# Performance work log

Hardware: AMD Instinct MI355X
Metric: run time of the kernel (lower is better)

Reference implementation:

```python
import jax, jax.numpy as jnp
import numpy as np

HEAD_COUNT = 16
HEAD_DIM = 128  # embed_count // head_count = 2048 // 16


def setup_inputs() -> dict:
    key = jax.random.key(0)
    k0, k1, k2, k3, k4 = jax.random.split(key, 5)
    B, C, S = 4, 2048, 1024
    keys = jax.random.normal(k0, (B, C, 1, S), dtype=jnp.float32)
    values = jax.random.normal(k1, (B, C, 1, S), dtype=jnp.float32)
    queries = jax.random.normal(k2, (B, C, 1, S), dtype=jnp.float32)
    attention_mask = jax.random.randint(k3, (B, S), 0, 2).astype(bool)
    # guarantee at least one valid key per batch row so softmax is finite
    attention_mask = attention_mask.at[:, 0].set(True)
    w_out = jax.random.normal(k4, (C, C), dtype=jnp.float32) * 0.02
    return {"keys": keys, "values": values, "queries": queries,
            "attention_mask": attention_mask, "w_out": w_out}


def reference(keys, values, queries, attention_mask, w_out):
    B, C, _, S = keys.shape
    h, d = HEAD_COUNT, HEAD_DIM
    # keys: [B,C,1,S] -> transpose(1,3) -> [B,S,1,C] -> [B,S,h,d]
    k = jnp.transpose(keys[:, :, 0, :], (0, 2, 1)).reshape(B, S, h, d)      # bkhd
    # values/queries: [B,C,1,S] -> [B,h,d,S] -> transpose(1,2) -> [B,d,h,S]
    v = jnp.transpose(values[:, :, 0, :].reshape(B, h, d, S), (0, 2, 1, 3))  # bdhk
    q = jnp.transpose(queries[:, :, 0, :].reshape(B, h, d, S), (0, 2, 1, 3)) # bdhq
    # additive mask bias: 0 where attended, -inf where masked; broadcast over h,q
    bias = jnp.where(attention_mask, 0.0, -jnp.inf).astype(keys.dtype)       # [B,K]
    scale = 1.0 / np.sqrt(d).astype(np.float32)
    w = jnp.einsum('bdhq,bkhd->bkhq', q * scale, k)                          # [B,K,h,Q]
    w = w + bias[:, :, None, None]
    w = jax.nn.softmax(w, axis=1)  # softmax over keys (dim 1)
    hid = jnp.einsum('bkhq,bdhk->bdhq', w, v)                                # [B,d,h,Q]
    hid = jnp.transpose(hid, (0, 2, 1, 3)).reshape(B, C, S)                  # [B,C,Q]
    out = jnp.einsum('oc,bcq->boq', w_out, hid)                              # 1x1 conv out_proj
    return out.reshape(B, C, 1, S)
```

## Files before the change

### kernel.cpp

```cpp
#include <hip/hip_runtime.h>

#define Bq 4
#define Cc 2048
#define Ss 1024
#define Hh 16
#define Dd 128

#define QSCALE 0.127517429f

typedef __bf16 bf16x8 __attribute__((ext_vector_type(8)));
typedef float  f32x4  __attribute__((ext_vector_type(4)));

__device__ __forceinline__ ushort f2bf(float f) {
    uint u = __float_as_uint(f);
    u += 0x7FFFu + ((u >> 16) & 1u);
    return (ushort)(u >> 16);
}
__device__ __forceinline__ uint pack2bf(float a, float b) {
    return (uint)f2bf(a) | ((uint)f2bf(b) << 16);
}
__device__ __forceinline__ void gld16(const void* g, void* l) {
    __builtin_amdgcn_global_load_lds(
        (const __attribute__((address_space(1))) unsigned int*)g,
        (__attribute__((address_space(3))) unsigned int*)l, 16, 0, 0);
}

__global__ __launch_bounds__(256) void prep_all(const float* __restrict__ w,
                                                const float* __restrict__ v,
                                                const float* __restrict__ keys,
                                                ushort* __restrict__ wb,
                                                ushort* __restrict__ vb,
                                                ushort* __restrict__ Kt) {
    __shared__ __align__(16) float T[128][65];
    const int t = threadIdx.x;
    const int blk = blockIdx.x;

    if (blk < 2048) {
        const size_t e = ((size_t)blk * 256 + t) * 8;
        const int row = (int)(e >> 11), col = (int)(e & 2047);
        const int colS = (col & ~63) | ((col & 63) ^ ((row & 7) << 3));
        float4 v0 = *(const float4*)&w[e];
        float4 v1 = *(const float4*)&w[e + 4];
        uint4 o;
        o.x = pack2bf(v0.x, v0.y); o.y = pack2bf(v0.z, v0.w);
        o.z = pack2bf(v1.x, v1.y); o.w = pack2bf(v1.z, v1.w);
        *(uint4*)&wb[(size_t)row * 2048 + colS] = o;
    } else if (blk < 6144) {
        const int tid = (blk - 2048) * 256 + t;
        const int row = tid >> 7;
        const int cp = tid & 127;
        const int blk64 = (cp >> 3) * 64;
        const int j0 = cp & 7;
        const int b5 = j0 >> 2, h = j0 & 3;
        const float* src = v + (size_t)row * 1024 + blk64 + 32 * b5 + 4 * h;
        float4 A = *(const float4*)src;
        float4 B = *(const float4*)(src + 16);
        uint4 o;
        o.x = pack2bf(A.x, A.y); o.y = pack2bf(A.z, A.w);
        o.z = pack2bf(B.x, B.y); o.w = pack2bf(B.z, B.w);
        *(uint4*)&vb[(size_t)row * 1024 + blk64 + ((j0 * 8) ^ ((row & 7) << 3))] = o;
    } else {
        const int b2 = blk - 6144;
        const int s0 = (b2 & 15) * 64;
        const int bh = b2 >> 4;
        const float* src = keys + (size_t)bh * 128 * 1024;
#pragma unroll
        for (int p = 0; p < 8; ++p) {
            const int d = p * 16 + (t >> 4);
            float4 v4 = *(const float4*)&src[(size_t)d * 1024 + s0 + (t & 15) * 4];
            T[d][(t & 15) * 4 + 0] = v4.x;
            T[d][(t & 15) * 4 + 1] = v4.y;
            T[d][(t & 15) * 4 + 2] = v4.z;
            T[d][(t & 15) * 4 + 3] = v4.w;
        }
        __syncthreads();
#pragma unroll
        for (int p = 0; p < 4; ++p) {
            const int k = p * 16 + (t >> 4);
            const int x = t & 15;
            uint4 o;
            o.x = pack2bf(T[x * 8 + 0][k], T[x * 8 + 1][k]);
            o.y = pack2bf(T[x * 8 + 2][k], T[x * 8 + 3][k]);
            o.z = pack2bf(T[x * 8 + 4][k], T[x * 8 + 5][k]);
            o.w = pack2bf(T[x * 8 + 6][k], T[x * 8 + 7][k]);
            const size_t rowbyte = ((size_t)bh * 1024 + s0 + k) * 256;
            const int boff = (x * 16) ^ ((k & 7) << 4);
            *(uint4*)((char*)Kt + rowbyte + boff) = o;
        }
    }
}

__global__ __launch_bounds__(512, 2) void attn7(const float* __restrict__ queries,
                                                const ushort* __restrict__ Kt,
                                                const ushort* __restrict__ Vbf,
                                                const unsigned* __restrict__ mask,
                                                ushort* __restrict__ hidT) {
    __shared__ __align__(16) char SMEM[102416];
    float* biasS = (float*)(SMEM + 98304);
    int* flg = (int*)(SMEM + 102400);

    const int t = threadIdx.x, l = t & 63, w = t >> 6;
    const int kk = l & 15, g = l >> 4;

    const int bid = blockIdx.x;
    const int vid = (bid & 7) * 32 + (bid >> 3);
    const int bh = vid >> 2, qt = vid & 3;
    const int b = bh >> 4, hh = bh & 15;
    const int q0 = qt * 256;
    const size_t bhbase = (size_t)bh * 1024;

    if (t == 0) { flg[0] = 0; flg[1] = 0; }
    __syncthreads();
    {
        int a = 0, c = 0;
        for (int i = t; i < 1024; i += 512) {
            unsigned vv = mask[i];
            if (vv != 0u && vv != 1u) a = 1;
            if (vv != 0u && vv != 0x3F800000u) c = 1;
        }
        if (a) atomicOr(&flg[0], 1);
        if (c) atomicOr(&flg[1], 1);
        __syncthreads();
        const int mode = flg[0] ? (flg[1] ? 1 : 2) : 0;
        const int* mi = (const int*)mask;
        const unsigned char* mb = (const unsigned char*)mask;
        const float* mf = (const float*)mask;
        for (int i = t; i < 1024; i += 512) {
            bool on;
            if (mode == 0)      on = (mi[b * 1024 + i] != 0);
            else if (mode == 1) on = (mb[b * 1024 + i] != 0);
            else                on = (mf[b * 1024 + i] != 0.0f);
            biasS[i] = on ? 0.0f : -1e30f;
        }
    }

    const float* Qb = queries + ((size_t)(b * Cc + hh * Dd)) * Ss;
    bf16x8 qf[2][4];
#pragma unroll
    for (int qs = 0; qs < 2; ++qs)
#pragma unroll
        for (int dc = 0; dc < 4; ++dc) {
            const int q = q0 + w * 32 + qs * 16 + kk;
            float v0 = Qb[(size_t)(dc * 32 + g * 8 + 0) * Ss + q];
            float v1 = Qb[(size_t)(dc * 32 + g * 8 + 1) * Ss + q];
            float v2 = Qb[(size_t)(dc * 32 + g * 8 + 2) * Ss + q];
            float v3 = Qb[(size_t)(dc * 32 + g * 8 + 3) * Ss + q];
            float v4 = Qb[(size_t)(dc * 32 + g * 8 + 4) * Ss + q];
            float v5 = Qb[(size_t)(dc * 32 + g * 8 + 5) * Ss + q];
            float v6 = Qb[(size_t)(dc * 32 + g * 8 + 6) * Ss + q];
            float v7 = Qb[(size_t)(dc * 32 + g * 8 + 7) * Ss + q];
            uint4 u;
            u.x = pack2bf(v0 * QSCALE, v1 * QSCALE);
            u.y = pack2bf(v2 * QSCALE, v3 * QSCALE);
            u.z = pack2bf(v4 * QSCALE, v5 * QSCALE);
            u.w = pack2bf(v6 * QSCALE, v7 * QSCALE);
            qf[qs][dc] = *(bf16x8*)&u;
        }

    float lrun[2] = {0.0f, 0.0f};
    f32x4 hacc[2][8];
#pragma unroll
    for (int qs = 0; qs < 2; ++qs)
#pragma unroll
        for (int i = 0; i < 8; ++i) hacc[qs][i] = (f32x4){0.f, 0.f, 0.f, 0.f};

#define ATTN_STAGE(bufi, cki)                                                   \
    {                                                                           \
        const int k0n = (cki) * 64;                                             \
        ushort* Kd = (ushort*)SMEM + (bufi) * 8192;                             \
        ushort* Vd = (ushort*)(SMEM + 49152) + (bufi) * 8192;                   \
        _Pragma("unroll")                                                       \
        for (int ii = 0; ii < 4; ++ii) {                                        \
            const int inst = ii * 8 + w;                                        \
            if (inst < 16) {                                                    \
                gld16(Kt + (bhbase + k0n + inst * 4 + (l >> 4)) * 128 +         \
                          (l & 15) * 8,                                         \
                      Kd + inst * 512);                                         \
            } else {                                                            \
                const int i2 = inst - 16;                                       \
                gld16(Vbf + ((size_t)bh * 128 + i2 * 8 + (l >> 3)) * 1024 +     \
                          k0n + (l & 7) * 8,                                    \
                      Vd + i2 * 512);                                           \
            }                                                                   \
        }                                                                       \
    }

#define ATTN_COMPUTE(bi, ck)                                                     \
    {                                                                            \
        const int k0 = (ck) * 64;                                                \
        const ushort* KTb = (const ushort*)SMEM + (bi) * 8192;                   \
        const ushort* Vsb = (const ushort*)(SMEM + 49152) + (bi) * 8192;         \
        f32x4 sc[2][4];                                                          \
        __builtin_amdgcn_s_setprio(1);                                           \
        _Pragma("unroll")                                                        \
        for (int ns = 0; ns < 4; ++ns) {                                         \
            const f32x4 ci = *(const f32x4*)&biasS[k0 + ns * 16 + g * 4];        \
            bf16x8 kf[4];                                                        \
            const ushort* kr = KTb + (ns * 16 + kk) * 128;                       \
            _Pragma("unroll")                                                    \
            for (int dc = 0; dc < 4; ++dc)                                       \
                kf[dc] = *(const bf16x8*)(kr +                                   \
                             ((dc * 32 + g * 8) ^ ((kk & 7) << 3)));             \
            _Pragma("unroll")                                                    \
            for (int qs = 0; qs < 2; ++qs) {                                     \
                f32x4 a = ci;                                                    \
                _Pragma("unroll")                                                \
                for (int dc = 0; dc < 4; ++dc)                                   \
                    a = __builtin_amdgcn_mfma_f32_16x16x32_bf16(                 \
                        kf[dc], qf[qs][dc], a, 0, 0, 0);                         \
                sc[qs][ns] = a;                                                  \
            }                                                                    \
        }                                                                        \
        __builtin_amdgcn_s_setprio(0);                                           \
        bf16x8 pb[2][2];                                                         \
        _Pragma("unroll")                                                        \
        for (int qs = 0; qs < 2; ++qs) {                                         \
            float pv[4][4];                                                      \
            float s = 0.0f;                                                      \
            _Pragma("unroll")                                                    \
            for (int ns = 0; ns < 4; ++ns) {                                     \
                _Pragma("unroll")                                                \
                for (int r = 0; r < 4; ++r) {                                    \
                    float p = exp2f(sc[qs][ns][r]);                              \
                    pv[ns][r] = p;                                               \
                    s += p;                                                      \
                }                                                                \
            }                                                                    \
            lrun[qs] += s;                                                       \
            _Pragma("unroll")                                                    \
            for (int kh = 0; kh < 2; ++kh) {                                     \
                bf16x8 vpk;                                                      \
                _Pragma("unroll")                                                \
                for (int j = 0; j < 8; ++j)                                      \
                    vpk[j] = (__bf16)pv[2 * kh + (j >> 2)][j & 3];               \
                pb[qs][kh] = vpk;                                                \
            }                                                                    \
        }                                                                        \
        __builtin_amdgcn_s_setprio(1);                                           \
        _Pragma("unroll")                                                        \
        for (int kh = 0; kh < 2; ++kh) {                                         \
            _Pragma("unroll")                                                    \
            for (int ds = 0; ds < 8; ++ds) {                                     \
                bf16x8 vf = *(const bf16x8*)(Vsb + (ds * 16 + kk) * 64 +         \
                                 ((kh * 32 + g * 8) ^ ((kk & 7) << 3)));         \
                hacc[0][ds] = __builtin_amdgcn_mfma_f32_16x16x32_bf16(           \
                    vf, pb[0][kh], hacc[0][ds], 0, 0, 0);                        \
                hacc[1][ds] = __builtin_amdgcn_mfma_f32_16x16x32_bf16(           \
                    vf, pb[1][kh], hacc[1][ds], 0, 0, 0);                        \
            }                                                                    \
        }                                                                        \
        __builtin_amdgcn_s_setprio(0);                                           \
    }

    ATTN_STAGE(0, 0);
    ATTN_STAGE(1, 1);
    asm volatile("s_waitcnt vmcnt(4)" ::: "memory");
    __builtin_amdgcn_s_barrier();

    int cb = 0, sb = 2;
    for (int ck = 0; ck < 14; ++ck) {
        ATTN_STAGE(sb, ck + 2);
        ATTN_COMPUTE(cb, ck);
        asm volatile("s_waitcnt vmcnt(4)" ::: "memory");
        __builtin_amdgcn_s_barrier();
        cb = (cb == 2) ? 0 : cb + 1;
        sb = (sb == 2) ? 0 : sb + 1;
    }
    ATTN_COMPUTE(cb, 14);
    asm volatile("s_waitcnt vmcnt(0)" ::: "memory");
    __builtin_amdgcn_s_barrier();
    cb = (cb == 2) ? 0 : cb + 1;
    ATTN_COMPUTE(cb, 15);
#undef ATTN_STAGE
#undef ATTN_COMPUTE

    float linv[2];
#pragma unroll
    for (int qs = 0; qs < 2; ++qs) {
        float s = lrun[qs];
        s += __shfl_xor(s, 16);
        s += __shfl_xor(s, 32);
        linv[qs] = 1.0f / s;
    }

    __syncthreads();
    {
        ushort* hs = (ushort*)SMEM;
#pragma unroll
        for (int qs = 0; qs < 2; ++qs) {
            const int row = w * 32 + qs * 16 + kk;
#pragma unroll
            for (int ds = 0; ds < 8; ++ds) {
                uint2 pk;
                pk.x = pack2bf(hacc[qs][ds][0] * linv[qs], hacc[qs][ds][1] * linv[qs]);
                pk.y = pack2bf(hacc[qs][ds][2] * linv[qs], hacc[qs][ds][3] * linv[qs]);
                const int off = row * 256 + ((ds * 32 + g * 8) ^ ((row & 7) << 4));
                *(uint2*)((char*)hs + off) = pk;
            }
        }
    }
    __syncthreads();

    const char* hsb = (const char*)SMEM;
#pragma unroll
    for (int it = 0; it < 8; ++it) {
        const int idx = it * 512 + t;
        const int q = idx >> 4, x = idx & 15;
        uint4 vv = *(const uint4*)(hsb + q * 256 + x * 16);
        *(uint4*)((char*)hidT + ((size_t)(b * Ss + q0 + q)) * 4096 + hh * 256 + x * 16) = vv;
    }
}

__global__ __launch_bounds__(512, 2) void proj5(const ushort* __restrict__ Wbf,
                                                const ushort* __restrict__ hidT,
                                                float* __restrict__ out) {
    __shared__ __align__(16) char SMEM[147456];
    const int t = threadIdx.x, l = t & 63, w = t >> 6;
    const int kk = l & 15, g = l >> 4;
    const int wr = w >> 2, wc = w & 3;

    const int bid = blockIdx.x;
    const int vid = (bid & 7) * 32 + (bid >> 3);
    const int o0 = (vid & 15) * 128;
    const int n0 = (vid >> 4) * 256;

    f32x4 acc[4][4];
#pragma unroll
    for (int i = 0; i < 4; ++i)
#pragma unroll
        for (int j = 0; j < 4; ++j) acc[i][j] = (f32x4){0.f, 0.f, 0.f, 0.f};

    const int swz = (kk & 7) << 3;

#define P5_STAGE_A(st, ks)                                                      \
    {                                                                           \
        ushort* Ad = (ushort*)SMEM + (st) * 8192;                               \
        _Pragma("unroll")                                                       \
        for (int ii = 0; ii < 2; ++ii) {                                        \
            const int idx = ii * 512 + t;                                       \
            gld16(Wbf + (size_t)(o0 + (idx >> 3)) * 2048 + (ks) * 64 +          \
                      (idx & 7) * 8,                                            \
                  Ad + idx * 8);                                                \
        }                                                                       \
    }
#define P5_STAGE_B(st, ks, p)                                                   \
    {                                                                           \
        ushort* Bd = (ushort*)(SMEM + 49152) + (st) * 16384;                    \
        _Pragma("unroll")                                                       \
        for (int jj = (p) * 2; jj < (p) * 2 + 2; ++jj) {                        \
            const int idx = jj * 512 + t;                                       \
            gld16(hidT + (size_t)(n0 + (idx >> 3)) * 2048 + (ks) * 64 +         \
                      (idx & 7) * 8,                                            \
                  Bd + idx * 8);                                                \
        }                                                                       \
    }
#define P5_READ(dcv)                                                            \
    _Pragma("unroll")                                                           \
    for (int ms = 0; ms < 4; ++ms)                                              \
        af[ms] = *(const bf16x8*)&Ab[(wr * 64 + ms * 16 + kk) * 64 +            \
                                     (((dcv) * 32 + g * 8) ^ swz)];             \
    _Pragma("unroll")                                                           \
    for (int ns = 0; ns < 4; ++ns)                                              \
        bfr[ns] = *(const bf16x8*)&Bb[(wc * 64 + ns * 16 + kk) * 64 +           \
                                      (((dcv) * 32 + g * 8) ^ swz)];
#define P5_MFMA()                                                               \
    __builtin_amdgcn_s_setprio(1);                                              \
    _Pragma("unroll")                                                           \
    for (int ms = 0; ms < 4; ++ms)                                              \
        _Pragma("unroll")                                                       \
        for (int ns = 0; ns < 4; ++ns)                                          \
            acc[ms][ns] = __builtin_amdgcn_mfma_f32_16x16x32_bf16(              \
                af[ms], bfr[ns], acc[ms][ns], 0, 0, 0);                         \
    __builtin_amdgcn_s_setprio(0);

    P5_STAGE_A(0, 0); P5_STAGE_B(0, 0, 0); P5_STAGE_B(0, 0, 1);
    P5_STAGE_A(1, 1); P5_STAGE_B(1, 1, 0); P5_STAGE_B(1, 1, 1);
    asm volatile("s_waitcnt vmcnt(6)" ::: "memory");
    __builtin_amdgcn_s_barrier();

    int ct = 0, st2 = 2;
    for (int tt = 0; tt < 32; ++tt) {
        const ushort* Ab = (const ushort*)SMEM + ct * 8192;
        const ushort* Bb = (const ushort*)(SMEM + 49152) + ct * 16384;
        bf16x8 af[4], bfr[4];

        P5_READ(0);
        if (tt < 30) { P5_STAGE_A(st2, tt + 2); P5_STAGE_B(st2, tt + 2, 0); }
        __builtin_amdgcn_s_barrier();
        asm volatile("s_waitcnt lgkmcnt(0)" ::: "memory");
        P5_MFMA();
        __builtin_amdgcn_s_barrier();

        P5_READ(1);
        if (tt < 30) P5_STAGE_B(st2, tt + 2, 1);
        if (tt < 30) { asm volatile("s_waitcnt vmcnt(6)" ::: "memory"); }
        else         { asm volatile("s_waitcnt vmcnt(0)" ::: "memory"); }
        __builtin_amdgcn_s_barrier();
        asm volatile("s_waitcnt lgkmcnt(0)" ::: "memory");
        P5_MFMA();
        __builtin_amdgcn_s_barrier();

        ct = (ct == 2) ? 0 : ct + 1;
        st2 = (st2 == 2) ? 0 : st2 + 1;
    }
#undef P5_STAGE_A
#undef P5_STAGE_B
#undef P5_READ
#undef P5_MFMA

#pragma unroll
    for (int ms = 0; ms < 4; ++ms)
#pragma unroll
        for (int ns = 0; ns < 4; ++ns) {
            const int o = o0 + wr * 64 + ms * 16 + g * 4;
            const int n = n0 + wc * 64 + ns * 16 + kk;
            const int bb = n >> 10, qq = n & 1023;
            float* op = out + ((size_t)(bb * Cc + o)) * Ss + qq;
#pragma unroll
            for (int r = 0; r < 4; ++r) op[(size_t)r * Ss] = acc[ms][ns][r];
        }
}

extern "C" void kernel_launch(void* const* d_in, const int* in_sizes, int n_in,
                              void* d_out, int out_size, void* d_ws, size_t ws_size,
                              hipStream_t stream) {
    const float*    keys    = (const float*)d_in[0];
    const float*    values  = (const float*)d_in[1];
    const float*    queries = (const float*)d_in[2];
    const unsigned* mask    = (const unsigned*)d_in[3];
    const float*    w_out   = (const float*)d_in[4];
    float* out = (float*)d_out;

    char* ws = (char*)d_ws;
    ushort* Wbf  = (ushort*)ws;
    ushort* Kt   = (ushort*)(ws + (8u << 20));
    ushort* Vbf  = (ushort*)(ws + (24u << 20));
    ushort* hidT = (ushort*)(ws + (40u << 20));

    hipLaunchKernelGGL(prep_all, dim3(7168), dim3(256), 0, stream,
                       w_out, values, keys, Wbf, Vbf, Kt);
    hipLaunchKernelGGL(attn7, dim3(256), dim3(512), 0, stream,
                       queries, Kt, Vbf, mask, hidT);
    hipLaunchKernelGGL(proj5, dim3(256), dim3(512), 0, stream,
                       Wbf, hidT, out);
}
```

Measured before the change: 114.8 us.

## Move Q transpose and mask bias into prep kernel, double-buffer attention

The prep kernel now also transposes, scales and converts queries to bf16 rows, and builds the additive mask bias once for all batches. The attention kernel reads Q fragments as contiguous 16-byte loads and copies the precomputed bias, so it no longer does strided fp32 query loads or mask-type detection per block. The K/V pipeline goes from triple to double buffering with a full vmcnt(0) wait each step, which shrinks LDS so launch bounds can allow more blocks per CU. In exchange the pipeline has less prefetch depth, and there is an extra Q round trip through global memory.

Result: slower. 194.8 us (+69.6%).

```diff
diff --git a/kernel.cpp b/kernel.cpp
--- a/kernel.cpp
+++ b/kernel.cpp
@@ -25,12 +25,16 @@
         (__attribute__((address_space(3))) unsigned int*)l, 16, 0, 0);
 }
 
-__global__ __launch_bounds__(256) void prep_all(const float* __restrict__ w,
-                                                const float* __restrict__ v,
-                                                const float* __restrict__ keys,
-                                                ushort* __restrict__ wb,
-                                                ushort* __restrict__ vb,
-                                                ushort* __restrict__ Kt) {
+__global__ __launch_bounds__(256) void prep_all2(const float* __restrict__ w,
+                                                 const float* __restrict__ v,
+                                                 const float* __restrict__ keys,
+                                                 const float* __restrict__ queries,
+                                                 const unsigned* __restrict__ mask,
+                                                 ushort* __restrict__ wb,
+                                                 ushort* __restrict__ vb,
+                                                 ushort* __restrict__ Kt,
+                                                 ushort* __restrict__ Qt,
+                                                 float* __restrict__ bias) {
     __shared__ __align__(16) float T[128][65];
     const int t = threadIdx.x;
     const int blk = blockIdx.x;
@@ -59,21 +63,24 @@
         o.x = pack2bf(A.x, A.y); o.y = pack2bf(A.z, A.w);
         o.z = pack2bf(B.x, B.y); o.w = pack2bf(B.z, B.w);
         *(uint4*)&vb[(size_t)row * 1024 + blk64 + ((j0 * 8) ^ ((row & 7) << 3))] = o;
-    } else {
-        const int b2 = blk - 6144;
+    } else if (blk < 8192) {
+        const int isQ = (blk >= 7168);
+        const int b2 = blk - (isQ ? 7168 : 6144);
         const int s0 = (b2 & 15) * 64;
         const int bh = b2 >> 4;
-        const float* src = keys + (size_t)bh * 128 * 1024;
+        const float* src = (isQ ? queries : keys) + (size_t)bh * 128 * 1024;
+        const float sc = isQ ? QSCALE : 1.0f;
 #pragma unroll
         for (int p = 0; p < 8; ++p) {
             const int d = p * 16 + (t >> 4);
             float4 v4 = *(const float4*)&src[(size_t)d * 1024 + s0 + (t & 15) * 4];
-            T[d][(t & 15) * 4 + 0] = v4.x;
-            T[d][(t & 15) * 4 + 1] = v4.y;
-            T[d][(t & 15) * 4 + 2] = v4.z;
-            T[d][(t & 15) * 4 + 3] = v4.w;
+            T[d][(t & 15) * 4 + 0] = v4.x * sc;
+            T[d][(t & 15) * 4 + 1] = v4.y * sc;
+            T[d][(t & 15) * 4 + 2] = v4.z * sc;
+            T[d][(t & 15) * 4 + 3] = v4.w * sc;
         }
         __syncthreads();
+        ushort* outp = isQ ? Qt : Kt;
 #pragma unroll
         for (int p = 0; p < 4; ++p) {
             const int k = p * 16 + (t >> 4);
@@ -84,20 +91,43 @@
             o.z = pack2bf(T[x * 8 + 4][k], T[x * 8 + 5][k]);
             o.w = pack2bf(T[x * 8 + 6][k], T[x * 8 + 7][k]);
             const size_t rowbyte = ((size_t)bh * 1024 + s0 + k) * 256;
-            const int boff = (x * 16) ^ ((k & 7) << 4);
-            *(uint4*)((char*)Kt + rowbyte + boff) = o;
-        }
-    }
-}
-
-__global__ __launch_bounds__(512, 2) void attn7(const float* __restrict__ queries,
+            const int boff = isQ ? (x * 16) : ((x * 16) ^ ((k & 7) << 4));
+            *(uint4*)((char*)outp + rowbyte + boff) = o;
+        }
+    } else {
+        __shared__ int f01, ff;
+        if (t == 0) { f01 = 0; ff = 0; }
+        __syncthreads();
+        int a = 0, c = 0;
+        for (int i = t; i < 1024; i += 256) {
+            unsigned vv = mask[i];
+            if (vv != 0u && vv != 1u) a = 1;
+            if (vv != 0u && vv != 0x3F800000u) c = 1;
+        }
+        if (a) atomicOr(&f01, 1);
+        if (c) atomicOr(&ff, 1);
+        __syncthreads();
+        const int mode = f01 ? (ff ? 1 : 2) : 0;
+        const int* mi = (const int*)mask;
+        const unsigned char* mb = (const unsigned char*)mask;
+        const float* mf = (const float*)mask;
+        for (int i = t; i < Bq * Ss; i += 256) {
+            bool on;
+            if (mode == 0)      on = (mi[i] != 0);
+            else if (mode == 1) on = (mb[i] != 0);
+            else                on = (mf[i] != 0.0f);
+            bias[i] = on ? 0.0f : -1e30f;
+        }
+    }
+}
+
+__global__ __launch_bounds__(512, 4) void attn8(const ushort* __restrict__ Qt,
                                                 const ushort* __restrict__ Kt,
                                                 const ushort* __restrict__ Vbf,
-                                                const unsigned* __restrict__ mask,
+                                                const float* __restrict__ bias,
                                                 ushort* __restrict__ hidT) {
-    __shared__ __align__(16) char SMEM[102416];
-    float* biasS = (float*)(SMEM + 98304);
-    int* flg = (int*)(SMEM + 102400);
+    __shared__ __align__(16) char SMEM[69632];
+    float* biasS = (float*)(SMEM + 65536);
 
     const int t = threadIdx.x, l = t & 63, w = t >> 6;
     const int kk = l & 15, g = l >> 4;
@@ -109,53 +139,16 @@
     const int q0 = qt * 256;
     const size_t bhbase = (size_t)bh * 1024;
 
-    if (t == 0) { flg[0] = 0; flg[1] = 0; }
-    __syncthreads();
-    {
-        int a = 0, c = 0;
-        for (int i = t; i < 1024; i += 512) {
-            unsigned vv = mask[i];
-            if (vv != 0u && vv != 1u) a = 1;
-            if (vv != 0u && vv != 0x3F800000u) c = 1;
-        }
-        if (a) atomicOr(&flg[0], 1);
-        if (c) atomicOr(&flg[1], 1);
-        __syncthreads();
-        const int mode = flg[0] ? (flg[1] ? 1 : 2) : 0;
-        const int* mi = (const int*)mask;
-        const unsigned char* mb = (const unsigned char*)mask;
-        const float* mf = (const float*)mask;
-        for (int i = t; i < 1024; i += 512) {
-            bool on;
-            if (mode == 0)      on = (mi[b * 1024 + i] != 0);
-            else if (mode == 1) on = (mb[b * 1024 + i] != 0);
-            else                on = (mf[b * 1024 + i] != 0.0f);
-            biasS[i] = on ? 0.0f : -1e30f;
-        }
-    }
-
-    const float* Qb = queries + ((size_t)(b * Cc + hh * Dd)) * Ss;
+    for (int i = t; i < Ss; i += 512) biasS[i] = bias[b * Ss + i];
+
     bf16x8 qf[2][4];
 #pragma unroll
-    for (int qs = 0; qs < 2; ++qs)
-#pragma unroll
-        for (int dc = 0; dc < 4; ++dc) {
-            const int q = q0 + w * 32 + qs * 16 + kk;
-            float v0 = Qb[(size_t)(dc * 32 + g * 8 + 0) * Ss + q];
-            float v1 = Qb[(size_t)(dc * 32 + g * 8 + 1) * Ss + q];
-            float v2 = Qb[(size_t)(dc * 32 + g * 8 + 2) * Ss + q];
-            float v3 = Qb[(size_t)(dc * 32 + g * 8 + 3) * Ss + q];
-            float v4 = Qb[(size_t)(dc * 32 + g * 8 + 4) * Ss + q];
-            float v5 = Qb[(size_t)(dc * 32 + g * 8 + 5) * Ss + q];
-            float v6 = Qb[(size_t)(dc * 32 + g * 8 + 6) * Ss + q];
-            float v7 = Qb[(size_t)(dc * 32 + g * 8 + 7) * Ss + q];
-            uint4 u;
-            u.x = pack2bf(v0 * QSCALE, v1 * QSCALE);
-            u.y = pack2bf(v2 * QSCALE, v3 * QSCALE);
-            u.z = pack2bf(v4 * QSCALE, v5 * QSCALE);
-            u.w = pack2bf(v6 * QSCALE, v7 * QSCALE);
-            qf[qs][dc] = *(bf16x8*)&u;
-        }
+    for (int qs = 0; qs < 2; ++qs) {
+        const ushort* qrow = Qt + (bhbase + q0 + w * 32 + qs * 16 + kk) * 128;
+#pragma unroll
+        for (int dc = 0; dc < 4; ++dc)
+            qf[qs][dc] = *(const bf16x8*)(qrow + dc * 32 + g * 8);
+    }
 
     float lrun[2] = {0.0f, 0.0f};
     f32x4 hacc[2][8];
@@ -168,7 +161,7 @@
     {                                                                           \
         const int k0n = (cki) * 64;                                             \
         ushort* Kd = (ushort*)SMEM + (bufi) * 8192;                             \
-        ushort* Vd = (ushort*)(SMEM + 49152) + (bufi) * 8192;                   \
+        ushort* Vd = (ushort*)(SMEM + 32768) + (bufi) * 8192;                   \
         _Pragma("unroll")                                                       \
         for (int ii = 0; ii < 4; ++ii) {                                        \
             const int inst = ii * 8 + w;                                        \
@@ -189,7 +182,7 @@
     {                                                                            \
         const int k0 = (ck) * 64;                                                \
         const ushort* KTb = (const ushort*)SMEM + (bi) * 8192;                   \
-        const ushort* Vsb = (const ushort*)(SMEM + 49152) + (bi) * 8192;         \
+        const ushort* Vsb = (const ushort*)(SMEM + 32768) + (bi) * 8192;         \
         f32x4 sc[2][4];                                                          \
         __builtin_amdgcn_s_setprio(1);                                           \
         _Pragma("unroll")                                                        \
@@ -253,24 +246,17 @@
     }
 
     ATTN_STAGE(0, 0);
-    ATTN_STAGE(1, 1);
-    asm volatile("s_waitcnt vmcnt(4)" ::: "memory");
-    __builtin_amdgcn_s_barrier();
-
-    int cb = 0, sb = 2;
-    for (int ck = 0; ck < 14; ++ck) {
-        ATTN_STAGE(sb, ck + 2);
-        ATTN_COMPUTE(cb, ck);
-        asm volatile("s_waitcnt vmcnt(4)" ::: "memory");
-        __builtin_amdgcn_s_barrier();
-        cb = (cb == 2) ? 0 : cb + 1;
-        sb = (sb == 2) ? 0 : sb + 1;
-    }
-    ATTN_COMPUTE(cb, 14);
     asm volatile("s_waitcnt vmcnt(0)" ::: "memory");
     __builtin_amdgcn_s_barrier();
-    cb = (cb == 2) ? 0 : cb + 1;
-    ATTN_COMPUTE(cb, 15);
+
+    int buf = 0;
+    for (int ck = 0; ck < 16; ++ck) {
+        if (ck + 1 < 16) ATTN_STAGE(buf ^ 1, ck + 1);
+        ATTN_COMPUTE(buf, ck);
+        asm volatile("s_waitcnt vmcnt(0)" ::: "memory");
+        __builtin_amdgcn_s_barrier();
+        buf ^= 1;
+    }
 #undef ATTN_STAGE
 #undef ATTN_COMPUTE
 
@@ -432,15 +418,18 @@
     float* out = (float*)d_out;
 
     char* ws = (char*)d_ws;
-    ushort* Wbf  = (ushort*)ws;
-    ushort* Kt   = (ushort*)(ws + (8u << 20));
-    ushort* Vbf  = (ushort*)(ws + (24u << 20));
-    ushort* hidT = (ushort*)(ws + (40u << 20));
-
-    hipLaunchKernelGGL(prep_all, dim3(7168), dim3(256), 0, stream,
-                       w_out, values, keys, Wbf, Vbf, Kt);
-    hipLaunchKernelGGL(attn7, dim3(256), dim3(512), 0, stream,
-                       queries, Kt, Vbf, mask, hidT);
+    float*  bias = (float*)ws;
+    ushort* Wbf  = (ushort*)(ws + 16384);
+    ushort* Kt   = (ushort*)(ws + 16384 + (8u << 20));
+    ushort* Qt   = (ushort*)(ws + 16384 + (24u << 20));
+    ushort* Vbf  = (ushort*)(ws + 16384 + (40u << 20));
+    ushort* hidT = (ushort*)(ws + 16384 + (56u << 20));
+
+    hipLaunchKernelGGL(prep_all2, dim3(8193), dim3(256), 0, stream,
+                       w_out, values, keys, queries, mask,
+                       Wbf, Vbf, Kt, Qt, bias);
+    hipLaunchKernelGGL(attn8, dim3(256), dim3(512), 0, stream,
+                       Qt, Kt, Vbf, bias, hidT);
     hipLaunchKernelGGL(proj5, dim3(256), dim3(512), 0, stream,
                        Wbf, hidT, out);
 }
```
